# Performance work log

Hardware: AMD Instinct MI355X
Metric: run time of the kernel (lower is better)

## Reference

```python
import jax, jax.numpy as jnp
import numpy as np

T_MAX = 16           # max target instance label (labels 1..T_MAX, 0 = background)
CCL_ITERS = 128      # fixed label-propagation iterations for connected components
S1 = 0.7310585786300049    # sigmoid(1.0)
SP0 = 0.6931471805599453   # softplus(0.0) = log 2
SP1 = 1.3132616875182228   # softplus(1.0)


def bce_dice(logits, target):
    # BCEDiceLoss: BCE-with-logits (mean) + soft dice on sigmoid probs
    p = jax.nn.sigmoid(logits)
    bce = jnp.mean(jax.nn.softplus(logits) - logits * target)
    inter = jnp.sum(p * target)
    dice = 1.0 - (2.0 * inter + 1.0) / (jnp.sum(p) + jnp.sum(target) + 1.0)
    return bce + dice


def connected_components(mask):
    # 4-connected components via iterative max-label propagation.
    # mask: [B,H,W] bool. Returns int32 label map; component id = max flat index in component + 1.
    B, H, W = mask.shape
    init = jnp.where(mask, jnp.arange(1, B * H * W + 1, dtype=jnp.int32).reshape(B, H, W), 0)

    def step(lab, _):
        up = jnp.pad(lab, ((0, 0), (1, 0), (0, 0)))[:, :H, :]
        dn = jnp.pad(lab, ((0, 0), (0, 1), (0, 0)))[:, 1:, :]
        lf = jnp.pad(lab, ((0, 0), (0, 0), (1, 0)))[:, :, :W]
        rt = jnp.pad(lab, ((0, 0), (0, 0), (0, 1)))[:, :, 1:]
        nb = jnp.maximum(jnp.maximum(up, dn), jnp.maximum(lf, rt))
        return jnp.where(mask, jnp.maximum(lab, nb), 0), None

    lab, _ = jax.lax.scan(step, init, None, length=CCL_ITERS)
    return lab


def _forward(pred_out, target_mask):
    B, C, H, W = pred_out.shape
    N = B * H * W
    Nf = jnp.float32(N)

    pm = jnp.argmax(pred_out, axis=1)          # [B,H,W] in {0,1} since C=2
    fg = pm > 0                                 # predicted foreground

    # base loss on channel-1 logits masked to predicted foreground vs binarized target
    res = bce_dice(pred_out[:, 1:2] * fg[:, None].astype(pred_out.dtype),
                   (target_mask > 0).astype(jnp.float32))

    # relabel predicted foreground into connected components (global unique ids)
    lab = connected_components(fg)              # [B,H,W]
    comp = jnp.where(fg, lab - 1, 0).reshape(-1)          # component root id in [0,N)
    tgt = target_mask[:, 0].reshape(-1).astype(jnp.int32)  # target label 0..T_MAX
    w = fg.reshape(-1).astype(jnp.float32)

    # confusion counts: inter[p, t] = |{pixels: pred comp p AND target label t}|
    inter = jax.ops.segment_sum(w, comp * (T_MAX + 1) + tgt,
                                num_segments=N * (T_MAX + 1)).reshape(N, T_MAX + 1)
    cnt_p = inter.sum(axis=1)                                       # [N] pred comp sizes
    cnt_t = jax.ops.segment_sum(jnp.ones((N,), jnp.float32), tgt,
                                num_segments=T_MAX + 1)             # [T+1] target sizes

    def pair_losses(inter_t, ct):
        # BCEDice between binary comp mask (as logits in {0,1}) and binary target mask,
        # expressed in closed form from the confusion counts.
        bce = (Nf * SP0 + cnt_p * (SP1 - SP0) - inter_t) / Nf
        sum_pt = 0.5 * ct + (S1 - 0.5) * inter_t
        sum_p = 0.5 * Nf + (S1 - 0.5) * cnt_p
        dice = 1.0 - (2.0 * sum_pt + 1.0) / (sum_p + ct + 1.0)
        return bce + dice

    def step(carry, t):
        used, acc, matched, un_tgt = carry
        ct = cnt_t[t]
        present = ct > 0
        avail = (cnt_p > 0) & (~used)
        any_avail = jnp.any(avail)
        losses = jnp.where(avail, pair_losses(inter[:, t], ct), jnp.inf)
        idx = jnp.argmin(losses)
        do = present & any_avail
        acc = acc + jnp.where(do, losses[idx], 0.0)
        used = used.at[idx].set(used[idx] | do)
        matched = matched + do.astype(jnp.float32)
        un_tgt = un_tgt + (present & (~any_avail)).astype(jnp.float32)
        return (used, acc, matched, un_tgt), None

    carry0 = (jnp.zeros((N,), bool), res, jnp.float32(0.0), jnp.float32(0.0))
    (used, acc, matched, un_tgt), _ = jax.lax.scan(step, carry0, jnp.arange(1, T_MAX + 1))

    n_pred = jnp.sum((cnt_p > 0).astype(jnp.float32))   # total pred components
    return acc + (n_pred - matched) + un_tgt            # penalties for unmatched comps/targets


def setup_inputs() -> dict:
    key = jax.random.key(0)
    k1, k2 = jax.random.split(key)
    pred_out = jax.random.normal(k1, (4, 2, 512, 512), dtype=jnp.float32)
    target_mask = jax.random.randint(k2, (4, 1, 512, 512), 0, 17, dtype=jnp.int32)
    return {"pred_out": pred_out, "target_mask": target_mask}


def reference(pred_out, target_mask):
    return _forward(pred_out, target_mask)
```

## Files before the change

kernel.cpp:

```cpp
#include <hip/hip_runtime.h>
#include <math.h>

#define HH 512
#define WW 512
#define HWSZ (HH * WW)
#define NB 4
#define NPIX (NB * HWSZ)
#define TMAX 16

#define CAP 131072
#define NPART 24
#define NBLK 1024
#define SMB 256
#define RSTRIDE 20
#define FLAGBIT 0x80000000u
#define POLLCAP (1 << 22)

#define TS 32
#define SEAMS 15
#define EDGES_PER_DIR (NB * SEAMS * HH)
#define NEDGES (2 * EDGES_PER_DIR)
#define BORDER_BLOCKS 64

struct Scalars {
  double sums[4];
  int cnt_t[TMAX + 1];
  int n_comp;
};

__device__ __forceinline__ float pair_loss(float cp, float it, float ctf) {
  const float Nf = (float)NPIX;
  float bce = (Nf * 0.69314718f + cp * 0.62011451f - it) / Nf;
  float sum_pt = 0.5f * ctf + 0.23105858f * it;
  float sum_p = 0.5f * Nf + 0.23105858f * cp;
  float dice = 1.0f - (2.0f * sum_pt + 1.0f) / (sum_p + ctf + 1.0f);
  return bce + dice;
}

__device__ __forceinline__ int chaseRO(const int* __restrict__ P, int x) {
  int p = P[x];
  while (p != x) { x = p; p = P[x]; }
  return x;
}
__device__ __forceinline__ int findRootH(int* P, int x) {
  int p = P[x];
  while (p != x) {
    int gp = P[p];
    if (gp == p) return p;
    P[x] = gp;
    x = gp; p = P[x];
  }
  return x;
}
__device__ void unite(int* P, int a, int b) {
  a = findRootH(P, a);
  b = findRootH(P, b);
  for (;;) {
    if (a == b) return;
    if (a > b) { int t = a; a = b; b = t; }
    int old = atomicMax(&P[a], b);
    if (old == a) return;
    a = findRootH(P, old);
    b = findRootH(P, b);
  }
}
__device__ __forceinline__ int findL(const int* lp, int x) {
  int p = lp[x];
  while (p != x) { x = p; p = lp[x]; }
  return x;
}
__device__ void uniteL(int* lp, int a, int b) {
  a = findL(lp, a);
  b = findL(lp, b);
  for (;;) {
    if (a == b) return;
    if (a > b) { int t = a; a = b; b = t; }
    int old = atomicMax(&lp[a], b);
    if (old == a) return;
    a = findL(lp, old);
    b = findL(lp, b);
  }
}

__global__ __launch_bounds__(256) void k_tile(const float* __restrict__ pred,
                                              const int* __restrict__ tgt,
                                              int* __restrict__ P,
                                              double* __restrict__ part,
                                              unsigned* __restrict__ state) {
  __shared__ int lp[TS * TS];
  __shared__ int hist[TMAX + 1];
  __shared__ double red[4][4];
  int tid = threadIdx.x, bid = blockIdx.x;
  if (!tid) state[bid] = 0;
  if (tid <= TMAX) hist[tid] = 0;
  int b = bid >> 8;
  int ty = (bid >> 4) & 15, tx = bid & 15;
  int gbase = b * HWSZ + ((ty << 5) << 9) + (tx << 5);
  int c0 = tid << 2;
  int hw0 = (gbase - b * HWSZ) + ((c0 >> 5) << 9) + (c0 & 31);
  int gi0 = b * HWSZ + hw0;
  const float* pb = pred + ((size_t)(b << 1)) * HWSZ;
  float4 p0 = *(const float4*)(pb + hw0);
  float4 p1 = *(const float4*)(pb + HWSZ + hw0);
  int4 tv = *(const int4*)(tgt + gi0);
  __syncthreads();

  float s0 = 0.f, s1 = 0.f, s2 = 0.f, s3 = 0.f;
#define ELEM(P0, P1, TV, K)                                      \
  {                                                              \
    bool fg = (P1) > (P0);                                       \
    float logit = fg ? (P1) : 0.0f;                              \
    float tb = ((TV) > 0) ? 1.0f : 0.0f;                         \
    float sp = fmaxf(logit, 0.0f) + log1pf(expf(-fabsf(logit))); \
    s0 += sp - logit * tb;                                       \
    float pr = 1.0f / (1.0f + expf(-logit));                     \
    s1 += pr; s2 += pr * tb; s3 += tb;                           \
    atomicAdd(&hist[TV], 1);                                     \
    lp[c0 + (K)] = fg ? (c0 + (K)) : -1;                         \
  }
  ELEM(p0.x, p1.x, tv.x, 0)
  ELEM(p0.y, p1.y, tv.y, 1)
  ELEM(p0.z, p1.z, tv.z, 2)
  ELEM(p0.w, p1.w, tv.w, 3)
#undef ELEM
  __syncthreads();

#pragma unroll
  for (int k = 0; k < 4; ++k) {
    int c = (k << 8) + tid;
    if (lp[c] >= 0) {
      int r = c >> 5, q = c & 31;
      if (q < TS - 1 && lp[c + 1] >= 0)  uniteL(lp, c, c + 1);
      if (r < TS - 1 && lp[c + TS] >= 0) uniteL(lp, c, c + TS);
    }
  }
  __syncthreads();
#pragma unroll
  for (int k = 0; k < 4; ++k) {
    int c = (k << 8) + tid;
    int gi = gbase + ((c >> 5) << 9) + (c & 31);
    if (lp[c] >= 0) {
      int rr = findL(lp, c);
      P[gi] = gbase + ((rr >> 5) << 9) + (rr & 31);
    } else {
      P[gi] = -1;
    }
  }

  for (int o = 32; o > 0; o >>= 1) {
    s0 += __shfl_down(s0, o);
    s1 += __shfl_down(s1, o);
    s2 += __shfl_down(s2, o);
    s3 += __shfl_down(s3, o);
  }
  int lane = tid & 63, wid = tid >> 6;
  if (!lane) { red[wid][0] = s0; red[wid][1] = s1; red[wid][2] = s2; red[wid][3] = s3; }
  __syncthreads();
  double* row = part + (size_t)bid * NPART;
  if (tid <= TMAX) row[4 + tid] = (double)hist[tid];
  if (!tid) {
    row[0] = red[0][0] + red[1][0] + red[2][0] + red[3][0];
    row[1] = red[0][1] + red[1][1] + red[2][1] + red[3][1];
    row[2] = red[0][2] + red[1][2] + red[2][2] + red[3][2];
    row[3] = red[0][3] + red[1][3] + red[2][3] + red[3][3];
  }
}

__global__ __launch_bounds__(256) void k_border(int* __restrict__ P,
                                                const double* __restrict__ part,
                                                Scalars* __restrict__ sc) {
  int tid = threadIdx.x;
  int bid = blockIdx.x;
  if (bid == 0) {
    int lane = tid & 63, wv = tid >> 6;
    double v[21];
#pragma unroll
    for (int j = 0; j < 21; ++j) v[j] = 0.0;
    for (int r = tid; r < NBLK; r += 256) {
      const double* row = part + (size_t)r * NPART;
#pragma unroll
      for (int j = 0; j < 21; ++j) v[j] += row[j];
    }
#pragma unroll
    for (int o = 32; o > 0; o >>= 1) {
#pragma unroll
      for (int j = 0; j < 21; ++j) v[j] += __shfl_down(v[j], o);
    }
    __shared__ double redr[4][21];
    if (!lane) {
#pragma unroll
      for (int j = 0; j < 21; ++j) redr[wv][j] = v[j];
    }
    __syncthreads();
    if (!tid) {
#pragma unroll
      for (int j = 0; j < 21; ++j) v[j] = redr[0][j] + redr[1][j] + redr[2][j] + redr[3][j];
      sc->sums[0] = v[0]; sc->sums[1] = v[1]; sc->sums[2] = v[2]; sc->sums[3] = v[3];
      for (int j = 0; j <= TMAX; ++j) sc->cnt_t[j] = (int)(v[4 + j] + 0.5);
    }
  }
  for (int e = bid * 256 + tid; e < NEDGES; e += BORDER_BLOCKS * 256) {
    int dir = e >= EDGES_PER_DIR;
    int e2 = dir ? e - EDGES_PER_DIR : e;
    int b = e2 / (SEAMS * HH);
    int r2 = e2 - b * (SEAMS * HH);
    int seam = r2 >> 9;
    int pos = r2 & 511;
    int i, j;
    if (!dir) {
      int w = (TS - 1) + (seam << 5);
      i = b * HWSZ + (pos << 9) + w;
      j = i + 1;
    } else {
      int h = (TS - 1) + (seam << 5);
      i = b * HWSZ + (h << 9) + pos;
      j = i + WW;
    }
    if (P[i] >= 0 && P[j] >= 0) unite(P, i, j);
  }
}

__global__ __launch_bounds__(256) void k_flatscan(int* __restrict__ P,
                                                  unsigned* __restrict__ state,
                                                  int* __restrict__ dof,
                                                  int* __restrict__ interD,
                                                  Scalars* __restrict__ sc) {
  __shared__ int redi[4];
  __shared__ int redp[4];
  __shared__ int wtot[4];
  int tid = threadIdx.x;
  int bid = blockIdx.x;
  int lane = tid & 63, wv = tid >> 6;
  int i0 = (bid << 10) + (tid << 2);
  int4 pv = *(const int4*)(P + i0);
  int4 rv;
  rv.x = (pv.x < 0) ? -1 : chaseRO(P, pv.x);
  rv.y = (pv.y < 0) ? -1 : chaseRO(P, pv.y);
  rv.z = (pv.z < 0) ? -1 : chaseRO(P, pv.z);
  rv.w = (pv.w < 0) ? -1 : chaseRO(P, pv.w);
  *(int4*)(P + i0) = rv;
  int isr[4] = { rv.x == i0 + 0, rv.y == i0 + 1, rv.z == i0 + 2, rv.w == i0 + 3 };
  int cme = isr[0] + isr[1] + isr[2] + isr[3];
  int c = cme;
  for (int o = 32; o > 0; o >>= 1) c += __shfl_down(c, o);
  if (!lane) redi[wv] = c;
  __syncthreads();
  int btot = redi[0] + redi[1] + redi[2] + redi[3];
  if (!tid) atomicExch(&state[bid], (unsigned)btot | FLAGBIT);

  int pre = 0;
  for (int j = tid; j < bid; j += 256) {
    unsigned v;
    int guard = 0;
    do { v = atomicAdd(&state[j], 0u); } while (!(v & FLAGBIT) && ++guard < POLLCAP);
    pre += (int)(v & 0x7FFFFFFFu);
  }
  for (int o = 32; o > 0; o >>= 1) pre += __shfl_down(pre, o);
  if (!lane) redp[wv] = pre;
  __syncthreads();
  int PRE = redp[0] + redp[1] + redp[2] + redp[3];
  if (bid == NBLK - 1 && !tid) sc->n_comp = PRE + btot;

  int v = cme;
  for (int o = 1; o < 64; o <<= 1) {
    int u = __shfl_up(v, o);
    if (lane >= o) v += u;
  }
  if (lane == 63) wtot[wv] = v;
  __syncthreads();
  int add = 0;
  for (int w = 0; w < wv; ++w) add += wtot[w];
  int d = PRE + v + add - cme;
#pragma unroll
  for (int k = 0; k < 4; ++k) {
    if (isr[k]) { dof[i0 + k] = d; ++d; }
  }
  size_t zs = (size_t)PRE * RSTRIDE;
  size_t ze = (size_t)(PRE + btot) * RSTRIDE;
  size_t zcap = (size_t)CAP * RSTRIDE;
  if (ze > zcap) ze = zcap;
  for (size_t j = zs + tid; j < ze; j += 256) interD[j] = 0;
}

__global__ __launch_bounds__(256) void k_interall(const int* __restrict__ P,
                                                  const int* __restrict__ tgt,
                                                  const int* __restrict__ dof,
                                                  int* __restrict__ interD) {
  int g = blockIdx.x * 256 + threadIdx.x;
  int i0 = g << 2;
  int4 rv = *(const int4*)(P + i0);
  int4 tv = *(const int4*)(tgt + i0);
#define DO(R, T)                                                     \
  if ((R) >= 0) {                                                    \
    int dd = dof[R];                                                 \
    if ((unsigned)dd < CAP) atomicAdd(&interD[(size_t)dd * RSTRIDE + (T)], 1); \
  }
  DO(rv.x, tv.x) DO(rv.y, tv.y) DO(rv.z, tv.z) DO(rv.w, tv.w)
#undef DO
}

__global__ __launch_bounds__(256) void k_scanmins(const Scalars* __restrict__ sc,
                                                  const int* __restrict__ interD,
                                                  unsigned long long* __restrict__ bm) {
  int tid = threadIdx.x;
  int n_comp = sc->n_comp;
  if (n_comp > CAP) n_comp = CAP;
  int d0 = (blockIdx.x << 9) + tid;
  int d1 = d0 + 256;
  int r0[RSTRIDE], r1[RSTRIDE];
  int cp0 = 0, cp1 = 0;
  if (d0 < n_comp) {
    const int4* rp = (const int4*)(interD + (size_t)d0 * RSTRIDE);
#pragma unroll
    for (int k = 0; k < 5; ++k) {
      int4 r4 = rp[k];
      r0[(k << 2) + 0] = r4.x; r0[(k << 2) + 1] = r4.y;
      r0[(k << 2) + 2] = r4.z; r0[(k << 2) + 3] = r4.w;
      cp0 += r4.x + r4.y + r4.z + r4.w;
    }
  }
  if (d1 < n_comp) {
    const int4* rp = (const int4*)(interD + (size_t)d1 * RSTRIDE);
#pragma unroll
    for (int k = 0; k < 5; ++k) {
      int4 r4 = rp[k];
      r1[(k << 2) + 0] = r4.x; r1[(k << 2) + 1] = r4.y;
      r1[(k << 2) + 2] = r4.z; r1[(k << 2) + 3] = r4.w;
      cp1 += r4.x + r4.y + r4.z + r4.w;
    }
  }
  __shared__ unsigned long long wmin[4][16];
  float cf0 = (float)cp0, cf1 = (float)cp1;
  int lane = tid & 63, wv = tid >> 6;
#pragma unroll
  for (int t = 1; t <= TMAX; ++t) {
    unsigned long long key = ~0ULL;
    float ctf = (float)sc->cnt_t[t];
    if (d0 < n_comp) {
      float loss = pair_loss(cf0, (float)r0[t], ctf);
      key = ((unsigned long long)__float_as_uint(loss) << 32) | (unsigned)d0;
    }
    if (d1 < n_comp) {
      float loss = pair_loss(cf1, (float)r1[t], ctf);
      unsigned long long k2 = ((unsigned long long)__float_as_uint(loss) << 32) | (unsigned)d1;
      if (k2 < key) key = k2;
    }
    for (int o = 32; o > 0; o >>= 1) {
      unsigned long long kk = __shfl_down(key, o);
      if (kk < key) key = kk;
    }
    if (!lane) wmin[wv][t - 1] = key;
  }
  __syncthreads();
  if (tid < 16) {
    unsigned long long m = wmin[0][tid];
    if (wmin[1][tid] < m) m = wmin[1][tid];
    if (wmin[2][tid] < m) m = wmin[2][tid];
    if (wmin[3][tid] < m) m = wmin[3][tid];
    bm[(size_t)tid * SMB + blockIdx.x] = m;
  }
}

__global__ __launch_bounds__(1024) void k_greedy(const Scalars* __restrict__ sc,
                                                 const int* __restrict__ interD,
                                                 const unsigned long long* __restrict__ bm,
                                                 float* __restrict__ out) {
  __shared__ unsigned long long lbm[16 * SMB];
  int tid = threadIdx.x;
  int lane = tid & 63;
#pragma unroll
  for (int k = 0; k < 4; ++k) lbm[tid + (k << 10)] = bm[tid + (k << 10)];
  __syncthreads();

  int n_comp = sc->n_comp;
  if (n_comp > CAP) n_comp = CAP;
  double acc = 0.0;
  int matched = 0, un = 0, nused = 0;
  int used_reg = -1;

  for (int t = 1; t <= TMAX; ++t) {
    int ct = sc->cnt_t[t];
    if (ct == 0) continue;
    const int rowoff = (t - 1) * SMB;
    for (int iter = 0; iter < 40; ++iter) {
      unsigned long long key = lbm[rowoff + lane];
#pragma unroll
      for (int k = 1; k < 4; ++k) {
        unsigned long long kk = lbm[rowoff + lane + (k << 6)];
        if (kk < key) key = kk;
      }
      for (int o = 32; o > 0; o >>= 1) {
        unsigned long long kk = __shfl_xor(key, o);
        if (kk < key) key = kk;
      }
      if (key == ~0ULL) { un += 1; break; }
      int dd = (int)(key & 0xFFFFFFFFu);
      bool ex = false;
      for (int u = 0; u < nused; ++u) {
        int uid = __shfl(used_reg, u);
        if (uid == dd) { ex = true; break; }
      }
      if (!ex) {
        acc += (double)__uint_as_float((unsigned)(key >> 32));
        matched += 1;
        if (lane == nused) used_reg = dd;
        nused += 1;
        break;
      }
      int b = dd >> 9;
      unsigned long long nk = ~0ULL;
#pragma unroll
      for (int k = 0; k < 8; ++k) {
        int d2 = (b << 9) + lane + (k << 6);
        if (d2 < n_comp) {
          bool ex2 = false;
          for (int u = 0; u < nused; ++u) {
            int uid = __shfl(used_reg, u);
            if (uid == d2) { ex2 = true; break; }
          }
          if (!ex2) {
            const int* rrow = interD + (size_t)d2 * RSTRIDE;
            int c = 0;
#pragma unroll
            for (int j = 0; j < RSTRIDE; ++j) c += rrow[j];
            float loss = pair_loss((float)c, (float)rrow[t], (float)ct);
            unsigned long long cand = ((unsigned long long)__float_as_uint(loss) << 32) | (unsigned)d2;
            if (cand < nk) nk = cand;
          }
        }
      }
      for (int o = 32; o > 0; o >>= 1) {
        unsigned long long kk = __shfl_xor(nk, o);
        if (kk < nk) nk = kk;
      }
      __syncthreads();
      if (!tid) lbm[rowoff + b] = nk;
      __syncthreads();
    }
  }

  if (!tid) {
    double Nd = (double)NPIX;
    double res = sc->sums[0] / Nd
               + 1.0 - (2.0 * sc->sums[2] + 1.0) / (sc->sums[1] + sc->sums[3] + 1.0);
    out[0] = (float)(res + acc + (double)(n_comp - matched) + (double)un);
  }
}

extern "C" void kernel_launch(void* const* d_in, const int* in_sizes, int n_in,
                              void* d_out, int out_size, void* d_ws, size_t ws_size,
                              hipStream_t stream) {
  (void)in_sizes; (void)n_in; (void)out_size; (void)ws_size;
  const float* pred = (const float*)d_in[0];
  const int* tgt = (const int*)d_in[1];
  float* out = (float*)d_out;

  char* w = (char*)d_ws;
  int* P     = (int*)w;            w += (size_t)NPIX * 4;
  int* dof   = (int*)w;            w += (size_t)NPIX * 4;
  double* part = (double*)w;       w += (size_t)NBLK * NPART * 8;
  Scalars* sc = (Scalars*)w;       w += 256;
  unsigned* state = (unsigned*)w;  w += 4096;
  unsigned long long* bm = (unsigned long long*)w; w += (size_t)16 * SMB * 8;
  int* interD = (int*)w;

  k_tile<<<NBLK, 256, 0, stream>>>(pred, tgt, P, part, state);
  k_border<<<BORDER_BLOCKS, 256, 0, stream>>>(P, part, sc);
  k_flatscan<<<NBLK, 256, 0, stream>>>(P, state, dof, interD, sc);
  k_interall<<<NBLK, 256, 0, stream>>>(P, tgt, dof, interD);
  k_scanmins<<<SMB, 256, 0, stream>>>(sc, interD, bm);
  k_greedy<<<1, 1024, 0, stream>>>(sc, interD, bm, out);
}
```

Measured before the change: 131.6 us.

## Split flatten-scan into two kernels to replace inter-block polling prefix

```diff
diff --git a/kernel.cpp b/kernel.cpp
--- a/kernel.cpp
+++ b/kernel.cpp
@@ -13,8 +13,6 @@
 #define NBLK 1024
 #define SMB 256
 #define RSTRIDE 20
-#define FLAGBIT 0x80000000u
-#define POLLCAP (1 << 22)
 
 #define TS 32
 #define SEAMS 15
@@ -85,13 +83,11 @@
 __global__ __launch_bounds__(256) void k_tile(const float* __restrict__ pred,
                                               const int* __restrict__ tgt,
                                               int* __restrict__ P,
-                                              double* __restrict__ part,
-                                              unsigned* __restrict__ state) {
+                                              double* __restrict__ part) {
   __shared__ int lp[TS * TS];
   __shared__ int hist[TMAX + 1];
   __shared__ double red[4][4];
   int tid = threadIdx.x, bid = blockIdx.x;
-  if (!tid) state[bid] = 0;
   if (tid <= TMAX) hist[tid] = 0;
   int b = bid >> 8;
   int ty = (bid >> 4) & 15, tx = bid & 15;
@@ -220,18 +216,12 @@
   }
 }
 
-__global__ __launch_bounds__(256) void k_flatscan(int* __restrict__ P,
-                                                  unsigned* __restrict__ state,
-                                                  int* __restrict__ dof,
-                                                  int* __restrict__ interD,
-                                                  Scalars* __restrict__ sc) {
+__global__ __launch_bounds__(256) void k_flatb(int* __restrict__ P,
+                                               int* __restrict__ bcnt) {
   __shared__ int redi[4];
-  __shared__ int redp[4];
-  __shared__ int wtot[4];
   int tid = threadIdx.x;
-  int bid = blockIdx.x;
-  int lane = tid & 63, wv = tid >> 6;
-  int i0 = (bid << 10) + (tid << 2);
+  int g = blockIdx.x * 256 + tid;
+  int i0 = g << 2;
   int4 pv = *(const int4*)(P + i0);
   int4 rv;
   rv.x = (pv.x < 0) ? -1 : chaseRO(P, pv.x);
@@ -239,28 +229,43 @@
   rv.z = (pv.z < 0) ? -1 : chaseRO(P, pv.z);
   rv.w = (pv.w < 0) ? -1 : chaseRO(P, pv.w);
   *(int4*)(P + i0) = rv;
+  int c = (rv.x == i0 + 0) + (rv.y == i0 + 1) + (rv.z == i0 + 2) + (rv.w == i0 + 3);
+  for (int o = 32; o > 0; o >>= 1) c += __shfl_down(c, o);
+  int lane = tid & 63, wv = tid >> 6;
+  if (!lane) redi[wv] = c;
+  __syncthreads();
+  if (!tid) bcnt[blockIdx.x] = redi[0] + redi[1] + redi[2] + redi[3];
+}
+
+__global__ __launch_bounds__(256) void k_scatter(const int* __restrict__ P,
+                                                 const int* __restrict__ bcnt,
+                                                 int* __restrict__ dof,
+                                                 int* __restrict__ interD,
+                                                 Scalars* __restrict__ sc) {
+  __shared__ int redi[4];
+  __shared__ int redp4[4];
+  __shared__ int wtot[4];
+  int tid = threadIdx.x;
+  int bid = blockIdx.x;
+  int lane = tid & 63, wv = tid >> 6;
+  int i0 = (bid << 10) + (tid << 2);
+  int4 rv = *(const int4*)(P + i0);
   int isr[4] = { rv.x == i0 + 0, rv.y == i0 + 1, rv.z == i0 + 2, rv.w == i0 + 3 };
   int cme = isr[0] + isr[1] + isr[2] + isr[3];
-  int c = cme;
-  for (int o = 32; o > 0; o >>= 1) c += __shfl_down(c, o);
-  if (!lane) redi[wv] = c;
-  __syncthreads();
-  int btot = redi[0] + redi[1] + redi[2] + redi[3];
-  if (!tid) atomicExch(&state[bid], (unsigned)btot | FLAGBIT);
-
-  int pre = 0;
-  for (int j = tid; j < bid; j += 256) {
-    unsigned v;
-    int guard = 0;
-    do { v = atomicAdd(&state[j], 0u); } while (!(v & FLAGBIT) && ++guard < POLLCAP);
-    pre += (int)(v & 0x7FFFFFFFu);
-  }
-  for (int o = 32; o > 0; o >>= 1) pre += __shfl_down(pre, o);
-  if (!lane) redp[wv] = pre;
-  __syncthreads();
-  int PRE = redp[0] + redp[1] + redp[2] + redp[3];
-  if (bid == NBLK - 1 && !tid) sc->n_comp = PRE + btot;
-
+  int4 bv = *(const int4*)(bcnt + (tid << 2));
+  int j0 = tid << 2;
+  int tot = bv.x + bv.y + bv.z + bv.w;
+  int pre = ((j0 + 0 < bid) ? bv.x : 0) + ((j0 + 1 < bid) ? bv.y : 0)
+          + ((j0 + 2 < bid) ? bv.z : 0) + ((j0 + 3 < bid) ? bv.w : 0);
+  for (int o = 32; o > 0; o >>= 1) {
+    tot += __shfl_down(tot, o);
+    pre += __shfl_down(pre, o);
+  }
+  if (!lane) { redi[wv] = tot; redp4[wv] = pre; }
+  __syncthreads();
+  tot = redi[0] + redi[1] + redi[2] + redi[3];
+  pre = redp4[0] + redp4[1] + redp4[2] + redp4[3];
+  if (bid == 0 && tid == 0) sc->n_comp = tot;
   int v = cme;
   for (int o = 1; o < 64; o <<= 1) {
     int u = __shfl_up(v, o);
@@ -270,13 +275,14 @@
   __syncthreads();
   int add = 0;
   for (int w = 0; w < wv; ++w) add += wtot[w];
-  int d = PRE + v + add - cme;
+  int d = pre + v + add - cme;
 #pragma unroll
   for (int k = 0; k < 4; ++k) {
     if (isr[k]) { dof[i0 + k] = d; ++d; }
   }
-  size_t zs = (size_t)PRE * RSTRIDE;
-  size_t ze = (size_t)(PRE + btot) * RSTRIDE;
+  int btot = wtot[0] + wtot[1] + wtot[2] + wtot[3];
+  size_t zs = (size_t)pre * RSTRIDE;
+  size_t ze = (size_t)(pre + btot) * RSTRIDE;
   size_t zcap = (size_t)CAP * RSTRIDE;
   if (ze > zcap) ze = zcap;
   for (size_t j = zs + tid; j < ze; j += 256) interD[j] = 0;
@@ -460,13 +466,14 @@
   int* dof   = (int*)w;            w += (size_t)NPIX * 4;
   double* part = (double*)w;       w += (size_t)NBLK * NPART * 8;
   Scalars* sc = (Scalars*)w;       w += 256;
-  unsigned* state = (unsigned*)w;  w += 4096;
+  int* bcnt  = (int*)w;            w += 4096;
   unsigned long long* bm = (unsigned long long*)w; w += (size_t)16 * SMB * 8;
   int* interD = (int*)w;
 
-  k_tile<<<NBLK, 256, 0, stream>>>(pred, tgt, P, part, state);
+  k_tile<<<NBLK, 256, 0, stream>>>(pred, tgt, P, part);
   k_border<<<BORDER_BLOCKS, 256, 0, stream>>>(P, part, sc);
-  k_flatscan<<<NBLK, 256, 0, stream>>>(P, state, dof, interD, sc);
+  k_flatb<<<NBLK, 256, 0, stream>>>(P, bcnt);
+  k_scatter<<<NBLK, 256, 0, stream>>>(P, bcnt, dof, interD, sc);
   k_interall<<<NBLK, 256, 0, stream>>>(P, tgt, dof, interD);
   k_scanmins<<<SMB, 256, 0, stream>>>(sc, interD, bm);
   k_greedy<<<1, 1024, 0, stream>>>(sc, interD, bm, out);
```

Result: faster. 124.4 us (-5.5%).
